# Kernel tuning notes

Measured on AMD Instinct MI355X. Metric: run time of the kernel, lower is better.

## Reference

```python
import jax, jax.numpy as jnp
import numpy as np

BATCH, T, N_STATES, EMIT = 128, 8192, 128, 64


def setup_inputs() -> dict:
    key = jax.random.key(0)
    kobs, kI, kA, kB = jax.random.split(key, 4)
    # one-hot observation sequences, as fed to the RNN cell
    obs = jax.random.randint(kobs, (BATCH, T), 0, EMIT)
    inputs = jax.nn.one_hot(obs, EMIT, dtype=jnp.float32)  # [B, T, EMIT]
    # valid probability parameters (model.I/A/B produce normalized matrices)
    I = jax.nn.softmax(jax.random.normal(kI, (N_STATES,), dtype=jnp.float32))
    A = jax.nn.softmax(jax.random.normal(kA, (N_STATES, N_STATES), dtype=jnp.float32), axis=-1)
    B = jax.nn.softmax(jax.random.normal(kB, (EMIT, N_STATES), dtype=jnp.float32), axis=0)
    return {"inputs": inputs, "I": I, "A": A, "B": B}


def reference(inputs, I, A, B):
    # HMM scaled forward algorithm, exactly the CgpHmmCell.call math,
    # run over the sequence with lax.scan (what keras.layers.RNN does step-wise).
    x = jnp.swapaxes(inputs, 0, 1)  # [T, batch, EMIT]

    # t == 0 (count == 1): R = I, Z = 1
    E0 = x[0] @ B                               # [batch, S]
    alpha0 = E0 * I[None, :]                    # [batch, S]
    loglik0 = jnp.log(jnp.sum(alpha0, axis=-1, keepdims=True))  # [batch, 1]

    def step(carry, x_t):
        alpha, loglik = carry
        Z = jnp.sum(alpha, axis=-1, keepdims=True)      # Z_{i-1}
        R = (alpha / Z) @ A                             # scaled forward @ A
        E = x_t @ B                                     # emission probs
        alpha_new = E * R
        loglik_new = loglik + jnp.log(jnp.sum(alpha_new, axis=-1, keepdims=True))
        return (alpha_new, loglik_new), None

    (alpha_f, loglik_f), _ = jax.lax.scan(step, (alpha0, loglik0), x[1:])
    return alpha_f, loglik_f
```

## Files before the change

kernel.cpp:

```cpp
#include <hip/hip_runtime.h>


#define BATCH 128
#define TLEN 8192
#define NS 128
#define EMIT 64
#define NCHUNK 512
#define CLEN (TLEN / NCHUNK)
#define WARM 8
#define BG 8
#define BSTR 132
#define LN64 4.158883083359672f

typedef __attribute__((ext_vector_type(8))) short short8;
typedef __attribute__((ext_vector_type(4))) float floatx4;
typedef __attribute__((ext_vector_type(4))) unsigned int uintx4;

__device__ __forceinline__ unsigned f2bf(float f) {
    return (__float_as_uint(f) + 0x8000u) >> 16;
}

__global__ __launch_bounds__(256) void decode_onehot(
        const floatx4* __restrict__ x, unsigned char* __restrict__ obsG,
        float* __restrict__ out_ll) {
    if (blockIdx.x == 0 && threadIdx.x < BATCH) out_ll[threadIdx.x] = 0.f;
    int i = blockIdx.x * 256 + threadIdx.x;
    floatx4 v = x[i];
    float s = v.x + v.y + v.z + v.w;
    if (s > 0.5f) {
        int e = (v.y > 0.5f) ? 1 : (v.z > 0.5f) ? 2 : (v.w > 0.5f) ? 3 : 0;
        int elem = (i << 2) + e;
        int row = elem >> 6;
        int col = elem & 63;
        int b = row >> 13;
        int t = row & (TLEN - 1);
        obsG[(b >> 4) * (16 * TLEN) + (b & 15) * TLEN + t] = (unsigned char)col;
    }
}

__global__ __launch_bounds__(64) void hmm_scan(
        const float* __restrict__ Amat,
        const float* __restrict__ Bmat,
        const float* __restrict__ Ivec,
        const unsigned char* __restrict__ obsG,
        float* __restrict__ out_alpha,
        float* __restrict__ out_ll)
{
    __shared__ unsigned short Bl[EMIT * BSTR];

    const int lane = threadIdx.x;
    const int n = lane & 15;
    const int q = lane >> 4;
    const int bg = blockIdx.x >> 9;
    const int c = blockIdx.x & (NCHUNK - 1);
    const bool first = (c == 0);
    const bool lastc = (c == NCHUNK - 1);
    const int steps = first ? CLEN : (CLEN + WARM);
    const int t0 = first ? 0 : c * CLEN - WARM;

    for (int i = lane; i < EMIT * NS; i += 64) {
        int e = i >> 7, col = i & (NS - 1);
        Bl[e * BSTR + col] = (unsigned short)f2bf(64.0f * Bmat[i]);
    }

    const unsigned char* orow = obsG + bg * (16 * TLEN) + n * TLEN;
    unsigned ow[6];
    if (first) {
        uintx4 a = *(const uintx4*)(orow);
        ow[0] = a.x; ow[1] = a.y; ow[2] = a.z; ow[3] = a.w;
        ow[4] = 0; ow[5] = 0;
    } else {
        uint2 a = *(const uint2*)(orow + t0);
        uintx4 b = *(const uintx4*)(orow + t0 + 8);
        ow[0] = a.x; ow[1] = a.y;
        ow[2] = b.x; ow[3] = b.y; ow[4] = b.z; ow[5] = b.w;
    }

    short8 af[8][4];
    #pragma unroll
    for (int mt = 0; mt < 8; ++mt)
        #pragma unroll
        for (int kf = 0; kf < 4; ++kf) {
            short8 v;
            #pragma unroll
            for (int j = 0; j < 8; ++j) {
                int u = 32 * kf + 8 * q + j;
                int sk = 32 * (u >> 5) + 16 * ((u >> 2) & 1)
                       + 4 * ((u >> 3) & 3) + (u & 3);
                v[j] = (short)f2bf(Amat[sk * NS + 16 * mt + n]);
            }
            af[mt][kf] = v;
        }
    __syncthreads();

    unsigned pk[16];
    #pragma unroll
    for (int i = 0; i < 16; ++i) pk[i] = 0x3C003C00u;

    float s_pre = 1.0f, s_penult = 1.0f, s_end = 1.0f;

    for (int it = 0; it < steps; ++it) {
        floatx4 acc[8];
        if (first && it == 0) {
            #pragma unroll
            for (int mt = 0; mt < 8; ++mt)
                acc[mt] = *(const floatx4*)(Ivec + 16 * mt + 4 * q);
        } else {
            short8 bf[4];
            #pragma unroll
            for (int kf = 0; kf < 4; ++kf) {
                uintx4 u4 = {pk[4 * kf], pk[4 * kf + 1], pk[4 * kf + 2], pk[4 * kf + 3]};
                bf[kf] = __builtin_bit_cast(short8, u4);
            }
            #pragma unroll
            for (int mt = 0; mt < 8; ++mt) {
                floatx4 a = {0.f, 0.f, 0.f, 0.f};
                #pragma unroll
                for (int kf = 0; kf < 4; ++kf)
                    a = __builtin_amdgcn_mfma_f32_16x16x32_bf16(af[mt][kf], bf[kf], a, 0, 0, 0);
                acc[mt] = a;
            }
        }

        int o = (ow[it >> 2] >> ((it & 3) * 8)) & 0xFF;
        int eb = o * BSTR;
        #pragma unroll
        for (int mt = 0; mt < 8; ++mt) {
            const unsigned* ep = (const unsigned*)(Bl + eb + 16 * mt + 4 * q);
            unsigned d0 = ep[0], d1 = ep[1];
            acc[mt].x *= __uint_as_float(d0 << 16);
            acc[mt].y *= __uint_as_float(d0 & 0xFFFF0000u);
            acc[mt].z *= __uint_as_float(d1 << 16);
            acc[mt].w *= __uint_as_float(d1 & 0xFFFF0000u);
        }

        bool need_red = (it == steps - 1) || (!first && it == WARM - 1) ||
                        (lastc && it == steps - 2);
        if (need_red) {
            float zz = 0.f;
            #pragma unroll
            for (int mt = 0; mt < 8; ++mt)
                zz += (acc[mt].x + acc[mt].y) + (acc[mt].z + acc[mt].w);
            zz += __shfl_xor(zz, 16, 64);
            zz += __shfl_xor(zz, 32, 64);
            if (it == steps - 1) s_end = zz;
            else if (lastc && it == steps - 2) s_penult = zz;
            else s_pre = zz;
        }

        if (lastc && it == steps - 1) {
            float inv = 1.0f / (64.0f * s_penult);
            #pragma unroll
            for (int mt = 0; mt < 8; ++mt) {
                floatx4 o4;
                o4.x = acc[mt].x * inv; o4.y = acc[mt].y * inv;
                o4.z = acc[mt].z * inv; o4.w = acc[mt].w * inv;
                *(floatx4*)(out_alpha + (bg * 16 + n) * NS + 16 * mt + 4 * q) = o4;
            }
        }

        #pragma unroll
        for (int mt = 0; mt < 8; ++mt) {
            unsigned u0 = __float_as_uint(acc[mt].x) + 0x8000u;
            unsigned u1 = __float_as_uint(acc[mt].y) + 0x8000u;
            unsigned u2 = __float_as_uint(acc[mt].z) + 0x8000u;
            unsigned u3 = __float_as_uint(acc[mt].w) + 0x8000u;
            pk[2 * mt]     = __builtin_amdgcn_perm(u1, u0, 0x07060302u);
            pk[2 * mt + 1] = __builtin_amdgcn_perm(u3, u2, 0x07060302u);
        }
    }

    if (q == 0) {
        float ll = __logf(s_end) - __logf(s_pre) - (float)CLEN * LN64;
        atomicAdd(&out_ll[bg * 16 + n], ll);
    }
}

extern "C" void kernel_launch(void* const* d_in, const int* in_sizes, int n_in,
                              void* d_out, int out_size, void* d_ws, size_t ws_size,
                              hipStream_t stream) {
    const float* x = (const float*)d_in[0];
    const float* I = (const float*)d_in[1];
    const float* A = (const float*)d_in[2];
    const float* B = (const float*)d_in[3];
    float* out = (float*)d_out;

    unsigned char* obsG = (unsigned char*)d_ws;

    decode_onehot<<<(BATCH * TLEN * 16) / 256, 256, 0, stream>>>(
        (const floatx4*)x, obsG, out + BATCH * NS);
    hmm_scan<<<BG * NCHUNK, 64, 0, stream>>>(A, B, I, obsG, out, out + BATCH * NS);
}
```

Baseline: 421.9 us.

## Fuse one-hot decode into scan via MFMA emission matmul, halve chunk count

Drops the separate one-hot decode kernel. The scan kernel now reads the float one-hot input directly and computes the emission probabilities with bf16 MFMA against register-resident B fragments, which removes the LDS table and its barrier. The chunk count goes from 512 to 256, so each chunk is longer and less time is spent on warm-up steps, at the cost of fewer blocks. The launch bound now allows two waves per SIMD. This adds 16 extra MFMAs and 64 bytes of input reads per lane every step, and it raises register pressure.

```diff
diff --git a/kernel.cpp b/kernel.cpp
--- a/kernel.cpp
+++ b/kernel.cpp
@@ -5,11 +5,10 @@
 #define TLEN 8192
 #define NS 128
 #define EMIT 64
-#define NCHUNK 512
+#define NCHUNK 256
 #define CLEN (TLEN / NCHUNK)
 #define WARM 8
 #define BG 8
-#define BSTR 132
 #define LN64 4.158883083359672f
 
 typedef __attribute__((ext_vector_type(8))) short short8;
@@ -20,61 +19,27 @@
     return (__float_as_uint(f) + 0x8000u) >> 16;
 }
 
-__global__ __launch_bounds__(256) void decode_onehot(
-        const floatx4* __restrict__ x, unsigned char* __restrict__ obsG,
-        float* __restrict__ out_ll) {
-    if (blockIdx.x == 0 && threadIdx.x < BATCH) out_ll[threadIdx.x] = 0.f;
-    int i = blockIdx.x * 256 + threadIdx.x;
-    floatx4 v = x[i];
-    float s = v.x + v.y + v.z + v.w;
-    if (s > 0.5f) {
-        int e = (v.y > 0.5f) ? 1 : (v.z > 0.5f) ? 2 : (v.w > 0.5f) ? 3 : 0;
-        int elem = (i << 2) + e;
-        int row = elem >> 6;
-        int col = elem & 63;
-        int b = row >> 13;
-        int t = row & (TLEN - 1);
-        obsG[(b >> 4) * (16 * TLEN) + (b & 15) * TLEN + t] = (unsigned char)col;
-    }
+__global__ void zero_ll(float* __restrict__ out_ll) {
+    out_ll[threadIdx.x] = 0.f;
 }
 
-__global__ __launch_bounds__(64) void hmm_scan(
+__global__ __launch_bounds__(64, 2) void hmm_scan(
+        const float* __restrict__ x,
         const float* __restrict__ Amat,
         const float* __restrict__ Bmat,
         const float* __restrict__ Ivec,
-        const unsigned char* __restrict__ obsG,
         float* __restrict__ out_alpha,
         float* __restrict__ out_ll)
 {
-    __shared__ unsigned short Bl[EMIT * BSTR];
-
     const int lane = threadIdx.x;
     const int n = lane & 15;
     const int q = lane >> 4;
-    const int bg = blockIdx.x >> 9;
+    const int bg = blockIdx.x >> 8;
     const int c = blockIdx.x & (NCHUNK - 1);
     const bool first = (c == 0);
     const bool lastc = (c == NCHUNK - 1);
     const int steps = first ? CLEN : (CLEN + WARM);
     const int t0 = first ? 0 : c * CLEN - WARM;
-
-    for (int i = lane; i < EMIT * NS; i += 64) {
-        int e = i >> 7, col = i & (NS - 1);
-        Bl[e * BSTR + col] = (unsigned short)f2bf(64.0f * Bmat[i]);
-    }
-
-    const unsigned char* orow = obsG + bg * (16 * TLEN) + n * TLEN;
-    unsigned ow[6];
-    if (first) {
-        uintx4 a = *(const uintx4*)(orow);
-        ow[0] = a.x; ow[1] = a.y; ow[2] = a.z; ow[3] = a.w;
-        ow[4] = 0; ow[5] = 0;
-    } else {
-        uint2 a = *(const uint2*)(orow + t0);
-        uintx4 b = *(const uintx4*)(orow + t0 + 8);
-        ow[0] = a.x; ow[1] = a.y;
-        ow[2] = b.x; ow[3] = b.y; ow[4] = b.z; ow[5] = b.w;
-    }
 
     short8 af[8][4];
     #pragma unroll
@@ -91,7 +56,27 @@
             }
             af[mt][kf] = v;
         }
-    __syncthreads();
+
+    short8 bfB[8][2];
+    #pragma unroll
+    for (int mt = 0; mt < 8; ++mt)
+        #pragma unroll
+        for (int kf = 0; kf < 2; ++kf) {
+            short8 v;
+            #pragma unroll
+            for (int j = 0; j < 8; ++j)
+                v[j] = (short)f2bf(64.0f * Bmat[(32 * kf + 8 * q + j) * NS + 16 * mt + n]);
+            bfB[mt][kf] = v;
+        }
+
+    floatx4 iv[8];
+    if (first) {
+        #pragma unroll
+        for (int mt = 0; mt < 8; ++mt)
+            iv[mt] = *(const floatx4*)(Ivec + 16 * mt + 4 * q);
+    }
+
+    const floatx4* xrow = (const floatx4*)x + (size_t)(bg * 16 + n) * (TLEN * 16);
 
     unsigned pk[16];
     #pragma unroll
@@ -100,38 +85,47 @@
     float s_pre = 1.0f, s_penult = 1.0f, s_end = 1.0f;
 
     for (int it = 0; it < steps; ++it) {
+        const floatx4* p = xrow + ((t0 + it) * 16 + 2 * q);
+        floatx4 x0 = p[0], x1 = p[1], x2 = p[8], x3 = p[9];
+        unsigned xw[4];
+        xw[0] = __builtin_amdgcn_perm(__float_as_uint(x0.y), __float_as_uint(x0.x), 0x07060302u);
+        xw[1] = __builtin_amdgcn_perm(__float_as_uint(x0.w), __float_as_uint(x0.z), 0x07060302u);
+        xw[2] = __builtin_amdgcn_perm(__float_as_uint(x1.y), __float_as_uint(x1.x), 0x07060302u);
+        xw[3] = __builtin_amdgcn_perm(__float_as_uint(x1.w), __float_as_uint(x1.z), 0x07060302u);
+        uintx4 xu0 = {xw[0], xw[1], xw[2], xw[3]};
+        xw[0] = __builtin_amdgcn_perm(__float_as_uint(x2.y), __float_as_uint(x2.x), 0x07060302u);
+        xw[1] = __builtin_amdgcn_perm(__float_as_uint(x2.w), __float_as_uint(x2.z), 0x07060302u);
+        xw[2] = __builtin_amdgcn_perm(__float_as_uint(x3.y), __float_as_uint(x3.x), 0x07060302u);
+        xw[3] = __builtin_amdgcn_perm(__float_as_uint(x3.w), __float_as_uint(x3.z), 0x07060302u);
+        uintx4 xu1 = {xw[0], xw[1], xw[2], xw[3]};
+        short8 xf0 = __builtin_bit_cast(short8, xu0);
+        short8 xf1 = __builtin_bit_cast(short8, xu1);
+
+        short8 bfa[4];
+        #pragma unroll
+        for (int kf = 0; kf < 4; ++kf) {
+            uintx4 u4 = {pk[4 * kf], pk[4 * kf + 1], pk[4 * kf + 2], pk[4 * kf + 3]};
+            bfa[kf] = __builtin_bit_cast(short8, u4);
+        }
+
+        const bool init0 = first && (it == 0);
         floatx4 acc[8];
-        if (first && it == 0) {
-            #pragma unroll
-            for (int mt = 0; mt < 8; ++mt)
-                acc[mt] = *(const floatx4*)(Ivec + 16 * mt + 4 * q);
-        } else {
-            short8 bf[4];
-            #pragma unroll
-            for (int kf = 0; kf < 4; ++kf) {
-                uintx4 u4 = {pk[4 * kf], pk[4 * kf + 1], pk[4 * kf + 2], pk[4 * kf + 3]};
-                bf[kf] = __builtin_bit_cast(short8, u4);
-            }
-            #pragma unroll
-            for (int mt = 0; mt < 8; ++mt) {
-                floatx4 a = {0.f, 0.f, 0.f, 0.f};
+        #pragma unroll
+        for (int mt = 0; mt < 8; ++mt) {
+            floatx4 e = {0.f, 0.f, 0.f, 0.f};
+            e = __builtin_amdgcn_mfma_f32_16x16x32_bf16(bfB[mt][0], xf0, e, 0, 0, 0);
+            e = __builtin_amdgcn_mfma_f32_16x16x32_bf16(bfB[mt][1], xf1, e, 0, 0, 0);
+            if (init0) {
+                acc[mt].x = e.x * iv[mt].x; acc[mt].y = e.y * iv[mt].y;
+                acc[mt].z = e.z * iv[mt].z; acc[mt].w = e.w * iv[mt].w;
+            } else {
+                floatx4 r = {0.f, 0.f, 0.f, 0.f};
                 #pragma unroll
                 for (int kf = 0; kf < 4; ++kf)
-                    a = __builtin_amdgcn_mfma_f32_16x16x32_bf16(af[mt][kf], bf[kf], a, 0, 0, 0);
-                acc[mt] = a;
+                    r = __builtin_amdgcn_mfma_f32_16x16x32_bf16(af[mt][kf], bfa[kf], r, 0, 0, 0);
+                acc[mt].x = e.x * r.x; acc[mt].y = e.y * r.y;
+                acc[mt].z = e.z * r.z; acc[mt].w = e.w * r.w;
             }
-        }
-
-        int o = (ow[it >> 2] >> ((it & 3) * 8)) & 0xFF;
-        int eb = o * BSTR;
-        #pragma unroll
-        for (int mt = 0; mt < 8; ++mt) {
-            const unsigned* ep = (const unsigned*)(Bl + eb + 16 * mt + 4 * q);
-            unsigned d0 = ep[0], d1 = ep[1];
-            acc[mt].x *= __uint_as_float(d0 << 16);
-            acc[mt].y *= __uint_as_float(d0 & 0xFFFF0000u);
-            acc[mt].z *= __uint_as_float(d1 << 16);
-            acc[mt].w *= __uint_as_float(d1 & 0xFFFF0000u);
         }
 
         bool need_red = (it == steps - 1) || (!first && it == WARM - 1) ||
@@ -185,9 +179,7 @@
     const float* B = (const float*)d_in[3];
     float* out = (float*)d_out;
 
-    unsigned char* obsG = (unsigned char*)d_ws;
-
-    decode_onehot<<<(BATCH * TLEN * 16) / 256, 256, 0, stream>>>(
-        (const floatx4*)x, obsG, out + BATCH * NS);
-    hmm_scan<<<BG * NCHUNK, 64, 0, stream>>>(A, B, I, obsG, out, out + BATCH * NS);
+    zero_ll<<<1, BATCH, 0, stream>>>(out + BATCH * NS);
+    hmm_scan<<<BG * NCHUNK, 64, 0, stream>>>(
+        x, A, B, I, out, out + BATCH * NS);
 }
```

Result: slower. 478.7 us (+13.5%).
